# Optimization experiments

Hardware: AMD Instinct MI355X
Metric: run time of the kernel (lower is better)

The kernel has to match this reference:

```python
import jax, jax.numpy as jnp
import numpy as np

HEADS = 8
DIM_HEAD = 64
DIM = 512
INNER = HEADS * DIM_HEAD  # 512
SCALE = DIM_HEAD ** -0.5


def setup_inputs() -> dict:
    key = jax.random.key(0)
    k1, k2, k3, k4 = jax.random.split(key, 4)
    b, n = 8, 4096
    x = jax.random.normal(k1, (b, n, DIM), dtype=jnp.float32)
    # torch Linear weight layout: [out_features, in_features]
    w_qkv = jax.random.normal(k2, (INNER * 3, DIM), dtype=jnp.float32) * (DIM ** -0.5)
    w_out = jax.random.normal(k3, (DIM, INNER), dtype=jnp.float32) * (INNER ** -0.5)
    b_out = jax.random.normal(k4, (DIM,), dtype=jnp.float32) * 0.01
    return {"x": x, "w_qkv": w_qkv, "w_out": w_out, "b_out": b_out}


def _feature_map(t):
    return jax.nn.elu(t) + 1.0


def reference(x, w_qkv, w_out, b_out):
    b, n, _ = x.shape
    h, d = HEADS, DIM_HEAD
    qkv = x @ w_qkv.T  # (b, n, 3*inner)
    q, k, v = jnp.split(qkv, 3, axis=-1)
    # (b, n, h*d) -> (b, h, n, d)
    reshape = lambda t: t.reshape(b, n, h, d).transpose(0, 2, 1, 3)
    q, k, v = reshape(q), reshape(k), reshape(v)
    q = _feature_map(q * SCALE)
    k = _feature_map(k)
    k_cumsum = k.sum(axis=2)  # (b, h, d)
    context = jnp.einsum('bhnd,bhne->bhde', k, v)
    out = jnp.einsum('bhnd,bhde->bhne', q, context)
    denom = jnp.einsum('bhnd,bhd->bhn', q, k_cumsum)[..., None] + 1e-8
    out = out / denom
    out = out.transpose(0, 2, 1, 3).reshape(b, n, h * d)
    return out @ w_out.T + b_out
```

## Files before the change

kernel.cpp:

```cpp
#include <hip/hip_runtime.h>
#include <cstdint>
#include <cstddef>

typedef __bf16 bf16_t;
typedef bf16_t bf16x8 __attribute__((ext_vector_type(8)));
typedef float f32x4 __attribute__((ext_vector_type(4)));
typedef unsigned short u16x8 __attribute__((ext_vector_type(8)));
typedef unsigned short u16x4 __attribute__((ext_vector_type(4)));

#define SEQ 4096
#define BATCH 8
#define NTOK 32768
#define NQKV 1536
#define DMODEL 512
#define NBH 64
#define NCHUNK 8

__device__ __forceinline__ unsigned short f2b(float f) {
    union { float f; unsigned u; } c; c.f = f;
    unsigned u = c.u;
    u += 0x7fffu + ((u >> 16) & 1u);
    return (unsigned short)(u >> 16);
}
__device__ __forceinline__ float b2f(unsigned short h) {
    union { unsigned u; float f; } c; c.u = ((unsigned)h) << 16;
    return c.f;
}
__device__ __forceinline__ float feat(float v) {
    return v > 0.f ? v + 1.f : __expf(v);
}

__device__ __forceinline__ void gload16(const unsigned short* g, unsigned short* lds_base) {
    __builtin_amdgcn_global_load_lds((const __attribute__((address_space(1))) unsigned int*)g,
                                     (__attribute__((address_space(3))) unsigned int*)lds_base,
                                     16, 0, 0);
}

__global__ __launch_bounds__(256) void prep_kernel(const float* __restrict__ x,
                                                   const float* __restrict__ wqkv,
                                                   const float* __restrict__ wout,
                                                   unsigned short* __restrict__ xB,
                                                   unsigned short* __restrict__ wqkvB,
                                                   unsigned short* __restrict__ woutB) {
    const int stride = gridDim.x * 256;
    const int t0 = blockIdx.x * 256 + threadIdx.x;
    for (int j = t0; j < NTOK * DMODEL / 4; j += stride) {
        f32x4 v = ((const f32x4*)x)[j];
        u16x4 o = { f2b(v[0]), f2b(v[1]), f2b(v[2]), f2b(v[3]) };
        ((u16x4*)xB)[j] = o;
    }
    for (int j = t0; j < NQKV * DMODEL / 4; j += stride) {
        f32x4 v = ((const f32x4*)wqkv)[j];
        u16x4 o = { f2b(v[0]), f2b(v[1]), f2b(v[2]), f2b(v[3]) };
        ((u16x4*)wqkvB)[j] = o;
    }
    for (int j = t0; j < DMODEL * DMODEL / 4; j += stride) {
        f32x4 v = ((const f32x4*)wout)[j];
        u16x4 o = { f2b(v[0]), f2b(v[1]), f2b(v[2]), f2b(v[3]) };
        ((u16x4*)woutB)[j] = o;
    }
}

template <int MODE>
__global__ __launch_bounds__(512) void gemm_kernel(const unsigned short* __restrict__ A,
                                                   const unsigned short* __restrict__ B,
                                                   void* __restrict__ Cq,
                                                   unsigned short* __restrict__ Ck,
                                                   unsigned short* __restrict__ Cv,
                                                   const float* __restrict__ bias,
                                                   int M, int N, int K, int nColBlocks) {
    __shared__ __align__(16) unsigned short As_[256 * 64];
    __shared__ __align__(16) unsigned short Bs_[128 * 64];
    const int tid = threadIdx.x;
    const int nwg = gridDim.x;
    int bid = blockIdx.x;
    if ((nwg & 7) == 0) bid = (bid & 7) * (nwg >> 3) + (bid >> 3);
    const int brow = bid / nColBlocks, bcol = bid % nColBlocks;
    const int rowBase = brow * 256, colBase = bcol * 128;
    const int lane = tid & 63, wv = tid >> 6;
    const int wm = wv >> 1, wn = wv & 1;
    const int lr = lane & 15, lk = lane >> 4;
    const int xorv = (lr & 7) << 4;
    const int sr8 = (wv << 3) + (lane >> 3);
    const int ss = lane & 7;

    f32x4 acc[4][4] = {};

    for (int kt = 0; kt < K; kt += 64) {
        #pragma unroll
        for (int j = 0; j < 4; ++j) {
            int r = j * 64 + sr8;
            int scol = ((ss ^ (r & 7)) << 3) + kt;
            gload16(A + (size_t)(rowBase + r) * K + scol, As_ + (j * 512 + (wv << 6)) * 8);
        }
        #pragma unroll
        for (int j = 0; j < 2; ++j) {
            int r = j * 64 + sr8;
            int scol = ((ss ^ (r & 7)) << 3) + kt;
            gload16(B + (size_t)(colBase + r) * K + scol, Bs_ + (j * 512 + (wv << 6)) * 8);
        }
        __syncthreads();
        #pragma unroll
        for (int kk = 0; kk < 2; ++kk) {
            bf16x8 af[4], bfr[4];
            #pragma unroll
            for (int mi = 0; mi < 4; ++mi) {
                int row = wm * 64 + mi * 16 + lr;
                af[mi] = *(const bf16x8*)((const char*)As_ + row * 128 + ((kk * 64 + lk * 16) ^ xorv));
            }
            #pragma unroll
            for (int ni = 0; ni < 4; ++ni) {
                int row = wn * 64 + ni * 16 + lr;
                bfr[ni] = *(const bf16x8*)((const char*)Bs_ + row * 128 + ((kk * 64 + lk * 16) ^ xorv));
            }
            #pragma unroll
            for (int mi = 0; mi < 4; ++mi)
                #pragma unroll
                for (int ni = 0; ni < 4; ++ni)
                    acc[mi][ni] = __builtin_amdgcn_mfma_f32_16x16x32_bf16(af[mi], bfr[ni], acc[mi][ni], 0, 0, 0);
        }
        __syncthreads();
    }

    if (MODE == 1) {
        #pragma unroll
        for (int mi = 0; mi < 4; ++mi) {
            const int grow0 = rowBase + wm * 64 + mi * 16 + lk * 4;
            #pragma unroll
            for (int ni = 0; ni < 4; ++ni) {
                const int gcol = colBase + wn * 64 + ni * 16 + lr;
                #pragma unroll
                for (int r = 0; r < 4; ++r)
                    ((float*)Cq)[(size_t)(grow0 + r) * DMODEL + gcol] = acc[mi][ni][r] + bias[gcol];
            }
        }
    } else if (colBase < 512) {
        #pragma unroll
        for (int mi = 0; mi < 4; ++mi) {
            const int grow0 = rowBase + wm * 64 + mi * 16 + lk * 4;
            #pragma unroll
            for (int ni = 0; ni < 4; ++ni) {
                const int gcol = colBase + wn * 64 + ni * 16 + lr;
                #pragma unroll
                for (int r = 0; r < 4; ++r)
                    ((unsigned short*)Cq)[(size_t)(grow0 + r) * DMODEL + gcol] =
                        f2b(feat(acc[mi][ni][r] * 0.125f));
            }
        }
    } else if (colBase < 1024) {
        #pragma unroll
        for (int mi = 0; mi < 4; ++mi) {
            const int grow0 = rowBase + wm * 64 + mi * 16 + lk * 4;
            const int b_ = grow0 >> 12, n0 = grow0 & 4095;
            #pragma unroll
            for (int ni = 0; ni < 4; ++ni) {
                const int hd = colBase - 512 + wn * 64 + ni * 16 + lr;
                u16x4 o = { f2b(feat(acc[mi][ni][0])), f2b(feat(acc[mi][ni][1])),
                            f2b(feat(acc[mi][ni][2])), f2b(feat(acc[mi][ni][3])) };
                *(u16x4*)&Ck[((size_t)(b_ * 512 + hd)) * SEQ + n0] = o;
            }
        }
    } else {
        #pragma unroll
        for (int mi = 0; mi < 4; ++mi) {
            const int grow0 = rowBase + wm * 64 + mi * 16 + lk * 4;
            const int b_ = grow0 >> 12, n0 = grow0 & 4095;
            #pragma unroll
            for (int ni = 0; ni < 4; ++ni) {
                const int hd = colBase - 1024 + wn * 64 + ni * 16 + lr;
                u16x4 o = { f2b(acc[mi][ni][0]), f2b(acc[mi][ni][1]),
                            f2b(acc[mi][ni][2]), f2b(acc[mi][ni][3]) };
                *(u16x4*)&Cv[((size_t)(b_ * 512 + hd)) * SEQ + n0] = o;
            }
        }
    }
}

__global__ __launch_bounds__(256) void ctx_kernel(const unsigned short* __restrict__ kT,
                                                  const unsigned short* __restrict__ vT,
                                                  float* __restrict__ ctxP,
                                                  float* __restrict__ kcP) {
    const int bh = blockIdx.x >> 3;
    const int chunk = blockIdx.x & 7;
    __shared__ __align__(16) unsigned short ks[64 * 64];
    __shared__ __align__(16) unsigned short vs[64 * 64];
    const int tid = threadIdx.x;
    const int lane = tid & 63, wv = tid >> 6;
    const int lr = lane & 15, lk = lane >> 4;
    const int xorv = (lr & 7) << 4;
    const int r_s = tid >> 3, s_s = tid & 7;
    const unsigned short* kg = kT + (size_t)bh * 64 * SEQ;
    const unsigned short* vg = vT + (size_t)bh * 64 * SEQ;

    f32x4 acc[4] = {};
    f32x4 kacc[4] = {};
    union { u16x8 u; bf16x8 b; } onesc;
    onesc.u = (u16x8){0x3F80, 0x3F80, 0x3F80, 0x3F80, 0x3F80, 0x3F80, 0x3F80, 0x3F80};
    const bf16x8 ones = onesc.b;

    for (int t = 0; t < 8; ++t) {
        const int n0 = chunk * 512 + t * 64;
        __syncthreads();
        #pragma unroll
        for (int j = 0; j < 2; ++j) {
            int r = j * 32 + r_s;
            int scol = ((s_s ^ (r & 7)) << 3) + n0;
            gload16(kg + (size_t)r * SEQ + scol, ks + (j * 256 + (wv << 6)) * 8);
            gload16(vg + (size_t)r * SEQ + scol, vs + (j * 256 + (wv << 6)) * 8);
        }
        __syncthreads();
        #pragma unroll
        for (int kk = 0; kk < 2; ++kk) {
            bf16x8 bfr = *(const bf16x8*)((const char*)vs + (wv * 16 + lr) * 128 + ((kk * 64 + lk * 16) ^ xorv));
            #pragma unroll
            for (int mi = 0; mi < 4; ++mi) {
                bf16x8 af = *(const bf16x8*)((const char*)ks + (mi * 16 + lr) * 128 + ((kk * 64 + lk * 16) ^ xorv));
                acc[mi] = __builtin_amdgcn_mfma_f32_16x16x32_bf16(af, bfr, acc[mi], 0, 0, 0);
                if (wv == 0)
                    kacc[mi] = __builtin_amdgcn_mfma_f32_16x16x32_bf16(af, ones, kacc[mi], 0, 0, 0);
            }
        }
    }
    float* cp = ctxP + ((size_t)chunk * NBH + bh) * 4096;
    #pragma unroll
    for (int mi = 0; mi < 4; ++mi)
        #pragma unroll
        for (int r = 0; r < 4; ++r)
            cp[(mi * 16 + lk * 4 + r) * 64 + wv * 16 + lr] = acc[mi][r];
    if (wv == 0 && lr == 0) {
        float* kp = kcP + ((size_t)chunk * NBH + bh) * 64;
        #pragma unroll
        for (int mi = 0; mi < 4; ++mi)
            #pragma unroll
            for (int r = 0; r < 4; ++r)
                kp[mi * 16 + lk * 4 + r] = kacc[mi][r];
    }
}

__global__ __launch_bounds__(256) void reduce_kernel(const float* __restrict__ ctxP,
                                                     const float* __restrict__ kcP,
                                                     unsigned short* __restrict__ cTh,
                                                     unsigned short* __restrict__ cTl,
                                                     float* __restrict__ kcR) {
    const int bh = blockIdx.x;
    const int t = threadIdx.x;
    #pragma unroll
    for (int p = 0; p < 4; ++p) {
        int idx = p * 256 + t;
        f32x4 s = {0.f, 0.f, 0.f, 0.f};
        for (int c = 0; c < NCHUNK; ++c)
            s += ((const f32x4*)(ctxP + ((size_t)c * NBH + bh) * 4096))[idx];
        int d = idx >> 4, e0 = (idx & 15) * 4;
        #pragma unroll
        for (int j = 0; j < 4; ++j) {
            unsigned short hi = f2b(s[j]);
            cTh[(size_t)bh * 4096 + (e0 + j) * 64 + d] = hi;
            cTl[(size_t)bh * 4096 + (e0 + j) * 64 + d] = f2b(s[j] - b2f(hi));
        }
    }
    if (t < 64) {
        float s = 0.f;
        for (int c = 0; c < NCHUNK; ++c) s += kcP[((size_t)c * NBH + bh) * 64 + t];
        kcR[bh * 64 + t] = s;
    }
}

__global__ __launch_bounds__(256) void attn_kernel(const unsigned short* __restrict__ qF,
                                                   const unsigned short* __restrict__ cTh,
                                                   const unsigned short* __restrict__ cTl,
                                                   const float* __restrict__ kcR,
                                                   unsigned short* __restrict__ inner) {
    const int bh = blockIdx.x >> 6;
    const int rt = blockIdx.x & 63;
    const int b = bh >> 3, h = bh & 7;
    const size_t rowBase = (size_t)b * SEQ + (size_t)rt * 64;
    __shared__ __align__(16) unsigned short qs[64 * 64];
    __shared__ __align__(16) unsigned short chs[64 * 64];
    __shared__ __align__(16) unsigned short cls[64 * 64];
    __shared__ float dpart[64][4];
    __shared__ float dens[64];
    __shared__ float kcs[64];
    const int tid = threadIdx.x;
    const int lane = tid & 63, wv = tid >> 6;
    const int lr = lane & 15, lk = lane >> 4;
    const int xorv = (lr & 7) << 4;
    const int r_s = tid >> 3, s_s = tid & 7;

    #pragma unroll
    for (int j = 0; j < 2; ++j) {
        int r = j * 32 + r_s;
        int sc = (s_s ^ (r & 7)) << 3;
        gload16(qF + (rowBase + r) * DMODEL + h * 64 + sc, qs + (j * 256 + (wv << 6)) * 8);
        gload16(cTh + (size_t)bh * 4096 + r * 64 + sc, chs + (j * 256 + (wv << 6)) * 8);
        gload16(cTl + (size_t)bh * 4096 + r * 64 + sc, cls + (j * 256 + (wv << 6)) * 8);
    }
    if (tid < 64) kcs[tid] = kcR[bh * 64 + tid];
    __syncthreads();
    {
        int row = tid & 63, part = tid >> 6;
        float s = 0.f;
        #pragma unroll
        for (int i = 0; i < 16; ++i) {
            int d = part * 16 + i;
            unsigned short qv = *(const unsigned short*)((const char*)qs + row * 128 + ((d * 2) ^ ((row & 7) << 4)));
            s += b2f(qv) * kcs[d];
        }
        dpart[row][part] = s;
    }
    __syncthreads();
    if (tid < 64) dens[tid] = 1e-8f + dpart[tid][0] + dpart[tid][1] + dpart[tid][2] + dpart[tid][3];
    __syncthreads();

    f32x4 acc[4] = {};
    #pragma unroll
    for (int kk = 0; kk < 2; ++kk) {
        bf16x8 af = *(const bf16x8*)((const char*)qs + (wv * 16 + lr) * 128 + ((kk * 64 + lk * 16) ^ xorv));
        #pragma unroll
        for (int ni = 0; ni < 4; ++ni) {
            bf16x8 bh_ = *(const bf16x8*)((const char*)chs + (ni * 16 + lr) * 128 + ((kk * 64 + lk * 16) ^ xorv));
            bf16x8 bl_ = *(const bf16x8*)((const char*)cls + (ni * 16 + lr) * 128 + ((kk * 64 + lk * 16) ^ xorv));
            acc[ni] = __builtin_amdgcn_mfma_f32_16x16x32_bf16(af, bh_, acc[ni], 0, 0, 0);
            acc[ni] = __builtin_amdgcn_mfma_f32_16x16x32_bf16(af, bl_, acc[ni], 0, 0, 0);
        }
    }
    #pragma unroll
    for (int ni = 0; ni < 4; ++ni)
        #pragma unroll
        for (int r = 0; r < 4; ++r) {
            int n = wv * 16 + lk * 4 + r;
            float o = acc[ni][r] / dens[n];
            inner[(rowBase + n) * DMODEL + h * 64 + ni * 16 + lr] = f2b(o);
        }
}

extern "C" void kernel_launch(void* const* d_in, const int* in_sizes, int n_in,
                              void* d_out, int out_size, void* d_ws, size_t ws_size,
                              hipStream_t stream) {
    (void)in_sizes; (void)n_in; (void)out_size; (void)ws_size;
    const float* x    = (const float*)d_in[0];
    const float* wqkv = (const float*)d_in[1];
    const float* wout = (const float*)d_in[2];
    const float* bout = (const float*)d_in[3];

    char* w = (char*)d_ws;
    unsigned short* xB    = (unsigned short*)(w);
    float*          ctxP  = (float*)(w);
    float*          kcP   = (float*)(w + 8388608);
    unsigned short* inner = (unsigned short*)(w);
    unsigned short* qF    = (unsigned short*)(w + 33554432);
    unsigned short* kT    = (unsigned short*)(w + 67108864);
    unsigned short* vT    = (unsigned short*)(w + 100663296);
    unsigned short* wqkvB = (unsigned short*)(w + 134217728);
    unsigned short* woutB = (unsigned short*)(w + 135790592);
    unsigned short* cTh   = (unsigned short*)(w + 136314880);
    unsigned short* cTl   = (unsigned short*)(w + 136839168);
    float*          kcR   = (float*)(w + 137363456);

    hipLaunchKernelGGL(prep_kernel, dim3(2048), dim3(256), 0, stream,
                       x, wqkv, wout, xB, wqkvB, woutB);
    hipLaunchKernelGGL((gemm_kernel<0>), dim3(1536), dim3(512), 0, stream,
                       xB, wqkvB, (void*)qF, kT, vT, (const float*)nullptr,
                       NTOK, NQKV, DMODEL, 12);
    hipLaunchKernelGGL(ctx_kernel, dim3(NBH * NCHUNK), dim3(256), 0, stream, kT, vT, ctxP, kcP);
    hipLaunchKernelGGL(reduce_kernel, dim3(NBH), dim3(256), 0, stream, ctxP, kcP, cTh, cTl, kcR);
    hipLaunchKernelGGL(attn_kernel, dim3(NBH * 64), dim3(256), 0, stream, qF, cTh, cTl, kcR, inner);
    hipLaunchKernelGGL((gemm_kernel<1>), dim3(512), dim3(512), 0, stream,
                       inner, woutB, (void*)d_out, (unsigned short*)nullptr, (unsigned short*)nullptr, bout,
                       NTOK, DMODEL, DMODEL, 4);
}
```

Baseline: 154.8 us.

## Prepack weights into MFMA fragment order and double-buffer A tiles in GEMM

The prep kernel now writes the bf16 weight matrices pre-swizzled into the exact per-lane MFMA fragment layout. The GEMM can then load B fragments straight from global memory into registers and skip LDS for B. The freed LDS holds a double buffer for the A tile, so the next tile's async global-to-LDS load overlaps the current MFMAs and one barrier per k-step is removed. This adds occupancy hints via launch_bounds(512,4), at the cost of per-lane global B loads inside the loop and a hardcoded K of 512.

```diff
diff --git a/kernel.cpp b/kernel.cpp
--- a/kernel.cpp
+++ b/kernel.cpp
@@ -15,6 +15,7 @@
 #define DMODEL 512
 #define NBH 64
 #define NCHUNK 8
+#define KSTEPS 8
 
 __device__ __forceinline__ unsigned short f2b(float f) {
     union { float f; unsigned u; } c; c.f = f;
@@ -36,12 +37,32 @@
                                      16, 0, 0);
 }
 
+__device__ __forceinline__ void packW(const float* __restrict__ src,
+                                      unsigned short* __restrict__ dst,
+                                      int totalP4, int t0, int stride) {
+    for (int j4 = t0; j4 < totalP4; j4 += stride) {
+        int p = j4 << 2;
+        int ke   = p & 7;
+        int lane = (p >> 3) & 63;
+        int ni   = (p >> 9) & 3;
+        int kk   = (p >> 11) & 1;
+        int wn   = (p >> 12) & 1;
+        int kt   = (p >> 13) & 7;
+        int bcol = p >> 16;
+        int n = bcol * 128 + wn * 64 + ni * 16 + (lane & 15);
+        int k = kt * 64 + kk * 32 + (lane >> 4) * 8 + ke;
+        f32x4 v = *(const f32x4*)&src[(size_t)n * 512 + k];
+        u16x4 o = { f2b(v[0]), f2b(v[1]), f2b(v[2]), f2b(v[3]) };
+        ((u16x4*)dst)[j4] = o;
+    }
+}
+
 __global__ __launch_bounds__(256) void prep_kernel(const float* __restrict__ x,
                                                    const float* __restrict__ wqkv,
                                                    const float* __restrict__ wout,
                                                    unsigned short* __restrict__ xB,
-                                                   unsigned short* __restrict__ wqkvB,
-                                                   unsigned short* __restrict__ woutB) {
+                                                   unsigned short* __restrict__ wqkvP,
+                                                   unsigned short* __restrict__ woutP) {
     const int stride = gridDim.x * 256;
     const int t0 = blockIdx.x * 256 + threadIdx.x;
     for (int j = t0; j < NTOK * DMODEL / 4; j += stride) {
@@ -49,28 +70,19 @@
         u16x4 o = { f2b(v[0]), f2b(v[1]), f2b(v[2]), f2b(v[3]) };
         ((u16x4*)xB)[j] = o;
     }
-    for (int j = t0; j < NQKV * DMODEL / 4; j += stride) {
-        f32x4 v = ((const f32x4*)wqkv)[j];
-        u16x4 o = { f2b(v[0]), f2b(v[1]), f2b(v[2]), f2b(v[3]) };
-        ((u16x4*)wqkvB)[j] = o;
-    }
-    for (int j = t0; j < DMODEL * DMODEL / 4; j += stride) {
-        f32x4 v = ((const f32x4*)wout)[j];
-        u16x4 o = { f2b(v[0]), f2b(v[1]), f2b(v[2]), f2b(v[3]) };
-        ((u16x4*)woutB)[j] = o;
-    }
+    packW(wqkv, wqkvP, NQKV * DMODEL / 4, t0, stride);
+    packW(wout, woutP, DMODEL * DMODEL / 4, t0, stride);
 }
 
 template <int MODE>
-__global__ __launch_bounds__(512) void gemm_kernel(const unsigned short* __restrict__ A,
-                                                   const unsigned short* __restrict__ B,
-                                                   void* __restrict__ Cq,
-                                                   unsigned short* __restrict__ Ck,
-                                                   unsigned short* __restrict__ Cv,
-                                                   const float* __restrict__ bias,
-                                                   int M, int N, int K, int nColBlocks) {
-    __shared__ __align__(16) unsigned short As_[256 * 64];
-    __shared__ __align__(16) unsigned short Bs_[128 * 64];
+__global__ __launch_bounds__(512, 4) void gemm_kernel(const unsigned short* __restrict__ A,
+                                                      const unsigned short* __restrict__ Bp,
+                                                      void* __restrict__ Cq,
+                                                      unsigned short* __restrict__ Ck,
+                                                      unsigned short* __restrict__ Cv,
+                                                      const float* __restrict__ bias,
+                                                      int M, int N, int K, int nColBlocks) {
+    __shared__ __align__(16) unsigned short As_[2][256 * 64];
     const int tid = threadIdx.x;
     const int nwg = gridDim.x;
     int bid = blockIdx.x;
@@ -86,40 +98,46 @@
 
     f32x4 acc[4][4] = {};
 
-    for (int kt = 0; kt < K; kt += 64) {
+    const unsigned short* bwl = Bp + ((size_t)bcol << 16) + ((size_t)wn << 12) + (lane << 3);
+
+    auto stageA = [&](int buf, int kt) {
         #pragma unroll
         for (int j = 0; j < 4; ++j) {
             int r = j * 64 + sr8;
             int scol = ((ss ^ (r & 7)) << 3) + kt;
-            gload16(A + (size_t)(rowBase + r) * K + scol, As_ + (j * 512 + (wv << 6)) * 8);
-        }
-        #pragma unroll
-        for (int j = 0; j < 2; ++j) {
-            int r = j * 64 + sr8;
-            int scol = ((ss ^ (r & 7)) << 3) + kt;
-            gload16(B + (size_t)(colBase + r) * K + scol, Bs_ + (j * 512 + (wv << 6)) * 8);
-        }
+            gload16(A + (size_t)(rowBase + r) * K + scol, &As_[buf][(j * 512 + (wv << 6)) * 8]);
+        }
+    };
+
+    stageA(0, 0);
+
+    #pragma unroll
+    for (int t = 0; t < KSTEPS; ++t) {
         __syncthreads();
+        bf16x8 bfr[2][4];
+        #pragma unroll
+        for (int kk = 0; kk < 2; ++kk)
+            #pragma unroll
+            for (int ni = 0; ni < 4; ++ni)
+                bfr[kk][ni] = *(const bf16x8*)(bwl + (t << 13) + (kk << 11) + (ni << 9));
+        __builtin_amdgcn_sched_barrier(0);
+        if (t + 1 < KSTEPS) stageA((t + 1) & 1, (t + 1) << 6);
+
+        const unsigned short* Ab = &As_[t & 1][0];
         #pragma unroll
         for (int kk = 0; kk < 2; ++kk) {
-            bf16x8 af[4], bfr[4];
+            bf16x8 af[4];
             #pragma unroll
             for (int mi = 0; mi < 4; ++mi) {
                 int row = wm * 64 + mi * 16 + lr;
-                af[mi] = *(const bf16x8*)((const char*)As_ + row * 128 + ((kk * 64 + lk * 16) ^ xorv));
-            }
-            #pragma unroll
-            for (int ni = 0; ni < 4; ++ni) {
-                int row = wn * 64 + ni * 16 + lr;
-                bfr[ni] = *(const bf16x8*)((const char*)Bs_ + row * 128 + ((kk * 64 + lk * 16) ^ xorv));
+                af[mi] = *(const bf16x8*)((const char*)Ab + row * 128 + ((kk * 64 + lk * 16) ^ xorv));
             }
             #pragma unroll
             for (int mi = 0; mi < 4; ++mi)
                 #pragma unroll
                 for (int ni = 0; ni < 4; ++ni)
-                    acc[mi][ni] = __builtin_amdgcn_mfma_f32_16x16x32_bf16(af[mi], bfr[ni], acc[mi][ni], 0, 0, 0);
-        }
-        __syncthreads();
+                    acc[mi][ni] = __builtin_amdgcn_mfma_f32_16x16x32_bf16(af[mi], bfr[kk][ni], acc[mi][ni], 0, 0, 0);
+        }
     }
 
     if (MODE == 1) {
@@ -350,21 +368,21 @@
     unsigned short* qF    = (unsigned short*)(w + 33554432);
     unsigned short* kT    = (unsigned short*)(w + 67108864);
     unsigned short* vT    = (unsigned short*)(w + 100663296);
-    unsigned short* wqkvB = (unsigned short*)(w + 134217728);
-    unsigned short* woutB = (unsigned short*)(w + 135790592);
+    unsigned short* wqkvP = (unsigned short*)(w + 134217728);
+    unsigned short* woutP = (unsigned short*)(w + 135790592);
     unsigned short* cTh   = (unsigned short*)(w + 136314880);
     unsigned short* cTl   = (unsigned short*)(w + 136839168);
     float*          kcR   = (float*)(w + 137363456);
 
     hipLaunchKernelGGL(prep_kernel, dim3(2048), dim3(256), 0, stream,
-                       x, wqkv, wout, xB, wqkvB, woutB);
+                       x, wqkv, wout, xB, wqkvP, woutP);
     hipLaunchKernelGGL((gemm_kernel<0>), dim3(1536), dim3(512), 0, stream,
-                       xB, wqkvB, (void*)qF, kT, vT, (const float*)nullptr,
+                       xB, wqkvP, (void*)qF, kT, vT, (const float*)nullptr,
                        NTOK, NQKV, DMODEL, 12);
     hipLaunchKernelGGL(ctx_kernel, dim3(NBH * NCHUNK), dim3(256), 0, stream, kT, vT, ctxP, kcP);
     hipLaunchKernelGGL(reduce_kernel, dim3(NBH), dim3(256), 0, stream, ctxP, kcP, cTh, cTl, kcR);
     hipLaunchKernelGGL(attn_kernel, dim3(NBH * 64), dim3(256), 0, stream, qF, cTh, cTl, kcR, inner);
     hipLaunchKernelGGL((gemm_kernel<1>), dim3(512), dim3(512), 0, stream,
-                       inner, woutB, (void*)d_out, (unsigned short*)nullptr, (unsigned short*)nullptr, bout,
+                       inner, woutP, (void*)d_out, (unsigned short*)nullptr, (unsigned short*)nullptr, bout,
                        NTOK, DMODEL, DMODEL, 4);
 }
```

After: 156.4 us. No clear change (+1.0%).
